# Kernel tuning notes

Measured on AMD Instinct MI355X. Metric: run time of the kernel, lower is better.

## Reference

```python
import jax, jax.numpy as jnp
import numpy as np

N, NJ, K, F = 30000, 12, 32, 128


def _resmlp(x, wr, br, w1, b1):
    # Residual: x + Linear(SiLU(x)); then ResMLP head: Linear(SiLU(.))
    h = x + jax.nn.silu(x) @ wr.T + br
    return jax.nn.silu(h) @ w1.T + b1


def setup_inputs() -> dict:
    key = jax.random.key(0)
    ks = jax.random.split(key, 40)
    d = {}
    d["atom_fea"] = jax.random.normal(ks[0], (N, F), jnp.float32)
    d["nbr_fea_idx"] = jax.random.randint(ks[1], (N, NJ), 0, N)
    d["gs"] = jax.random.normal(ks[2], (N, NJ, K), jnp.float32)
    d["gp"] = jax.random.normal(ks[3], (N, NJ, K, 3), jnp.float32)
    d["gd"] = jax.random.normal(ks[4], (N, NJ, K, 5), jnp.float32)
    # parameters (nn.init.uniform_ default is U[0,1); scaled down for stability)
    d["Gs"] = jax.random.uniform(ks[5], (F, K), jnp.float32) * 0.1
    d["Gp"] = jax.random.uniform(ks[6], (F, K), jnp.float32) * 0.1
    d["Gd"] = jax.random.uniform(ks[7], (F, K), jnp.float32) * 0.1
    d["P1"] = jax.random.uniform(ks[8], (F, F), jnp.float32) * 0.02
    d["P2"] = jax.random.uniform(ks[9], (F, F), jnp.float32) * 0.02
    d["D1"] = jax.random.uniform(ks[10], (F, F), jnp.float32) * 0.02
    d["D2"] = jax.random.uniform(ks[11], (F, F), jnp.float32) * 0.02
    i = 12
    for name in ("c", "s", "p", "d"):
        d[name + "_wr"] = jax.random.normal(ks[i], (F, F), jnp.float32) * 0.05; i += 1
        d[name + "_br"] = jnp.zeros((F,), jnp.float32)
        d[name + "_w1"] = jax.random.normal(ks[i], (F, F), jnp.float32) * 0.05; i += 1
        d[name + "_b1"] = jnp.zeros((F,), jnp.float32)
    return d


def reference(atom_fea, nbr_fea_idx, gs, gp, gd,
              Gs, Gp, Gd, P1, P2, D1, D2,
              c_wr, c_br, c_w1, c_b1,
              s_wr, s_br, s_w1, s_b1,
              p_wr, p_br, p_w1, p_b1,
              d_wr, d_br, d_w1, d_b1):
    s_fea = _resmlp(atom_fea, s_wr, s_br, s_w1, s_b1)  # (N,F)
    p_fea = _resmlp(atom_fea, p_wr, p_br, p_w1, p_b1)
    d_fea = _resmlp(atom_fea, d_wr, d_br, d_w1, d_b1)

    # s channel: env_j = Gs @ gs_j, si = sum_j s_fea[nbr_j] * env_j
    env_s = jnp.einsum('fk,njk->njf', Gs, gs)                 # (N,NJ,F)
    final_s = jnp.sum(s_fea[nbr_fea_idx] * env_s, axis=1)     # (N,F)

    # p channel: (N,F,3) per-atom, then trace((P2^T p^T)(p P1)) = sum(pP1 * pP2)
    env_p = jnp.einsum('fk,njka->njfa', Gp, gp)               # (N,NJ,F,3)
    all_p = jnp.sum(p_fea[nbr_fea_idx][..., None] * env_p, axis=1)  # (N,F,3)
    all_p = jnp.swapaxes(all_p, 1, 2)                          # (N,3,F)
    p1 = jnp.einsum('naf,fg->nag', all_p, P1)
    p2 = jnp.einsum('naf,fg->nag', all_p, P2)
    final_p = jnp.sum(p1 * p2, axis=(1, 2))[:, None]           # (N,1) -> bcast (N,F)

    # d channel: same with 5 components
    env_d = jnp.einsum('fk,njka->njfa', Gd, gd)               # (N,NJ,F,5)
    all_d = jnp.sum(d_fea[nbr_fea_idx][..., None] * env_d, axis=1)  # (N,F,5)
    all_d = jnp.swapaxes(all_d, 1, 2)                          # (N,5,F)
    d1 = jnp.einsum('naf,fg->nag', all_d, D1)
    d2 = jnp.einsum('naf,fg->nag', all_d, D2)
    final_d = jnp.sum(d1 * d2, axis=(1, 2))[:, None]

    final_c = _resmlp(atom_fea, c_wr, c_br, c_w1, c_b1)        # (N,F)
    return final_c + final_s + final_p + final_d
```

## Files before the change

kernel.cpp:

```cpp
#include <hip/hip_runtime.h>

#define N_ATOMS 30000
#define NJ 12
#define FDIM 128

typedef __attribute__((ext_vector_type(8))) short short8;
typedef __attribute__((ext_vector_type(4))) float f32x4;

#define WFRAG_OFF 0
#define GFRAG_OFF 262144
#define MFRAG_OFF 286720
#define FEA_OFF   483328
#define FEA_ELEMS 3840000
#define ALLP_OFF  23523328
#define ALLD_OFF  46563328
#define QP_OFF    84963328
#define QD_OFF    85323328

__device__ __forceinline__ unsigned pack_bf2(float a, float b){
  unsigned r;
  asm("v_cvt_pk_bf16_f32 %0, %1, %2" : "=v"(r) : "v"(a), "v"(b));
  return r;
}
__device__ __forceinline__ unsigned short f2b(float f){
  return (unsigned short)pack_bf2(f, 0.f);
}
__device__ __forceinline__ float b2f(unsigned short s){
  unsigned u = ((unsigned)s) << 16;
  return __builtin_bit_cast(float, u);
}
__device__ __forceinline__ float silu_f(float x){ return x / (1.0f + __expf(-x)); }
__device__ __forceinline__ void lds_fence(){
  __builtin_amdgcn_sched_barrier(0);
  asm volatile("s_waitcnt lgkmcnt(0)" ::: "memory");
  __builtin_amdgcn_sched_barrier(0);
}
__device__ __forceinline__ short8 frag4(unsigned d0, unsigned d1, unsigned d2, unsigned d3, bool valid){
  if (!valid){ d0 = 0u; d1 = 0u; d2 = 0u; d3 = 0u; }
  uint4 u; u.x = d0; u.y = d1; u.z = d2; u.w = d3;
  return __builtin_bit_cast(short8, u);
}

struct Ptr8 { const float* p[8]; };
struct Ptr3 { const float* p[3]; };
struct Bias { const float* br[4]; const float* b1[4]; };

__global__ __launch_bounds__(256) void k_prep(
    const float* __restrict__ P1, const float* __restrict__ P2,
    const float* __restrict__ D1, const float* __restrict__ D2,
    Ptr8 w8, Ptr3 g3, char* __restrict__ ws)
{
  int b = blockIdx.x, t = threadIdx.x;
  if (b < 16){
    int mat = b >> 3, rb = b & 7;
    const float* A = mat ? D1 : P1;
    const float* B = mat ? D2 : P2;
    unsigned short* dst = (unsigned short*)(ws + MFRAG_OFF) + (size_t)mat*16384;
    for (int it = 0; it < 8; ++it){
      int o = it*256 + t;
      int row = rb*16 + (o >> 7), col = o & 127;
      const float4* ar = (const float4*)(A + (size_t)row*128);
      const float4* br = (const float4*)(B + (size_t)col*128);
      float s = 0.f;
      #pragma unroll 8
      for (int q = 0; q < 32; ++q){
        float4 a = ar[q], c = br[q];
        s += a.x*c.x + a.y*c.y + a.z*c.z + a.w*c.w;
      }
      int ks = row >> 5, ft = col >> 4;
      int ln = (col & 15) | (((row >> 3) & 3) << 4);
      dst[(size_t)(((ks*8 + ft)*64 + ln)*8 + (row & 7))] = f2b(s);
    }
  } else if (b < 24){
    int mat = b - 16;
    const float* W = w8.p[mat];
    unsigned short* dst = (unsigned short*)(ws + WFRAG_OFF) + (size_t)mat*16384;
    for (int it = 0; it < 64; ++it){
      int idx = it*256 + t;
      int i = idx & 7, ln = (idx >> 3) & 63, ft = (idx >> 9) & 7, ks = idx >> 12;
      int f = ft*16 + (ln & 15);
      int k = ks*32 + ((ln >> 4) & 3)*8 + i;
      dst[idx] = f2b(W[(size_t)f*128 + k]);
    }
  } else {
    int mat = b - 24;
    const float* G = g3.p[mat];
    unsigned short* dst = (unsigned short*)(ws + GFRAG_OFF) + (size_t)mat*4096;
    for (int it = 0; it < 16; ++it){
      int idx = it*256 + t;
      int i = idx & 7, ln = (idx >> 3) & 63, ft = idx >> 9;
      int f = ft*16 + (ln & 15);
      int k = ((ln >> 4) & 3)*8 + i;
      dst[idx] = f2b(G[(size_t)f*32 + k]);
    }
  }
}

__global__ __launch_bounds__(256) void k_resmlp(
    const float* __restrict__ x, char* __restrict__ ws, Bias bs,
    float* __restrict__ out)
{
  __shared__ alignas(16) char sm[32768];
  const int tid = threadIdx.x, lane = tid & 63;
  const int wid = __builtin_amdgcn_readfirstlane(tid >> 6);
  const int lo = lane & 15, hi = lane >> 4;
  const int ch = blockIdx.y;
  const int rowbase = (int)blockIdx.x*64 + wid*16;
  char* xL = sm + wid*8192;
  char* hL = xL + 4096;

  #pragma unroll
  for (int it = 0; it < 8; ++it){
    int e4 = it*64 + lane;
    int row = e4 >> 5, k0 = (e4 & 31)*4;
    int grow = rowbase + row; if (grow >= N_ATOMS) grow = N_ATOMS-1;
    float4 v = *(const float4*)(x + (size_t)grow*FDIM + k0);
    uint2 u;
    u.x = pack_bf2(silu_f(v.x), silu_f(v.y));
    u.y = pack_bf2(silu_f(v.z), silu_f(v.w));
    int ks = k0 >> 5, h2 = (k0 >> 3) & 3, i0 = k0 & 7, lanep = row | (h2 << 4);
    *(uint2*)(xL + ks*1024 + lanep*16 + i0*2) = u;
  }
  lds_fence();
  short8 A[4];
  #pragma unroll
  for (int ks = 0; ks < 4; ++ks) A[ks] = *(const short8*)(xL + ks*1024 + lane*16);

  const char* wrp = ws + (size_t)(ch*2)*32768;
  const char* w1p = ws + (size_t)(ch*2 + 1)*32768;
  const float* brp = bs.br[ch];
  const float* b1p = bs.b1[ch];

  f32x4 acc[8];
  #pragma unroll
  for (int ft = 0; ft < 8; ++ft) acc[ft] = (f32x4){0.f,0.f,0.f,0.f};
  #pragma unroll
  for (int ks = 0; ks < 4; ++ks){
    #pragma unroll
    for (int ft = 0; ft < 8; ++ft){
      short8 B = *(const short8*)(wrp + (size_t)(((ks*8 + ft)*64 + lane)*16));
      acc[ft] = __builtin_amdgcn_mfma_f32_16x16x32_bf16(A[ks], B, acc[ft], 0, 0, 0);
    }
  }
  #pragma unroll
  for (int ft = 0; ft < 8; ++ft){
    int f = ft*16 + lo;
    float bias = brp[f];
    #pragma unroll
    for (int r = 0; r < 4; ++r){
      int grow = rowbase + hi*4 + r; if (grow >= N_ATOMS) grow = N_ATOMS-1;
      float h = acc[ft][r] + x[(size_t)grow*FDIM + f] + bias;
      float sh = silu_f(h);
      int ks2 = f >> 5, h2 = (f >> 3) & 3, i2 = f & 7, lanep = (hi*4 + r) | (h2 << 4);
      *(unsigned short*)(hL + ks2*1024 + lanep*16 + i2*2) = f2b(sh);
    }
  }
  lds_fence();
  short8 A2[4];
  #pragma unroll
  for (int ks = 0; ks < 4; ++ks) A2[ks] = *(const short8*)(hL + ks*1024 + lane*16);

  f32x4 acc2[8];
  #pragma unroll
  for (int ft = 0; ft < 8; ++ft) acc2[ft] = (f32x4){0.f,0.f,0.f,0.f};
  #pragma unroll
  for (int ks = 0; ks < 4; ++ks){
    #pragma unroll
    for (int ft = 0; ft < 8; ++ft){
      short8 B = *(const short8*)(w1p + (size_t)(((ks*8 + ft)*64 + lane)*16));
      acc2[ft] = __builtin_amdgcn_mfma_f32_16x16x32_bf16(A2[ks], B, acc2[ft], 0, 0, 0);
    }
  }
  if (ch == 0){
    #pragma unroll
    for (int ft = 0; ft < 8; ++ft){
      int f = ft*16 + lo;
      float bb = b1p[f];
      #pragma unroll
      for (int r = 0; r < 4; ++r){
        int grow = rowbase + hi*4 + r; if (grow >= N_ATOMS) grow = N_ATOMS-1;
        out[(size_t)grow*FDIM + f] = acc2[ft][r] + bb;
      }
    }
  } else {
    unsigned short* fea = (unsigned short*)(ws + FEA_OFF) + (size_t)(ch-1)*FEA_ELEMS;
    #pragma unroll
    for (int ft = 0; ft < 8; ++ft){
      int f = ft*16 + lo;
      float bb = b1p[f];
      #pragma unroll
      for (int r = 0; r < 4; ++r){
        int grow = rowbase + hi*4 + r; if (grow >= N_ATOMS) grow = N_ATOMS-1;
        fea[(size_t)grow*FDIM + f] = f2b(acc2[ft][r] + bb);
      }
    }
  }
}

#define FPAD 264
#define SLAB 4224

__device__ __forceinline__ void stage_fea(char* buf, const unsigned short* fea,
                                          int nb, int lane)
{
  #pragma unroll
  for (int j = 0; j < NJ; ++j){
    int nj = __builtin_amdgcn_readlane(nb, j);
    const unsigned* rp = (const unsigned*)(fea + (size_t)nj*FDIM);
    unsigned v = rp[lane];
    *(unsigned*)(buf + j*FPAD + lane*4) = v;
  }
}

__device__ __forceinline__ void body_s(
    const float* __restrict__ gs, const int* __restrict__ nbr,
    char* __restrict__ ws, float* __restrict__ out,
    char* feaL, int atom, int lane, int lo, int hi, int jc, bool jvalid)
{
  const unsigned short* feaS = (const unsigned short*)(ws + FEA_OFF);
  const f32x4 z4 = {0.f,0.f,0.f,0.f};
  int nb = 0;
  if (lane < NJ) nb = nbr[(size_t)atom*NJ + lane];

  const float* gsp = gs + (size_t)atom*384 + (jc*32 + hi*8);
  f32x4 v0 = *(const f32x4*)(gsp);
  f32x4 v1 = *(const f32x4*)(gsp + 4);

  stage_fea(feaL, feaS, nb, lane);

  short8 AfS = frag4(pack_bf2(v0[0],v0[1]), pack_bf2(v0[2],v0[3]),
                     pack_bf2(v1[0],v1[1]), pack_bf2(v1[2],v1[3]), jvalid);
  short8 Bg[8];
  #pragma unroll
  for (int ft = 0; ft < 8; ++ft)
    Bg[ft] = *(const short8*)(ws + GFRAG_OFF + (size_t)((ft*64 + lane)*16));

  const char* a0 = feaL + hi*(4*FPAD) + lo*2;

  lds_fence();
  float outv0 = 0.f, outv1 = 0.f;
  #pragma unroll
  for (int ft = 0; ft < 8; ++ft){
    float w0 = b2f(*(const unsigned short*)(a0 + 0*FPAD + ft*32));
    float w1 = b2f(*(const unsigned short*)(a0 + 1*FPAD + ft*32));
    float w2 = b2f(*(const unsigned short*)(a0 + 2*FPAD + ft*32));
    float w3 = b2f(*(const unsigned short*)(a0 + 3*FPAD + ft*32));
    f32x4 c = __builtin_amdgcn_mfma_f32_16x16x32_bf16(AfS, Bg[ft], z4, 0, 0, 0);
    float p = c[0]*w0 + c[1]*w1 + c[2]*w2 + c[3]*w3;
    p += __shfl_xor(p, 16);
    p += __shfl_xor(p, 32);
    if (ft == hi)     outv0 += p;
    if (ft == hi + 4) outv1 += p;
  }
  size_t ob = (size_t)atom*FDIM;
  out[ob + lane]      += outv0;
  out[ob + 64 + lane] += outv1;
}

__device__ __forceinline__ void body_p(
    const float* __restrict__ gp, const int* __restrict__ nbr,
    char* __restrict__ ws,
    char* feaL, int atom, int lane, int lo, int hi, int jc, bool jvalid)
{
  const unsigned short* feaP = (const unsigned short*)(ws + FEA_OFF) + FEA_ELEMS;
  unsigned short* allp = (unsigned short*)(ws + ALLP_OFF);
  const f32x4 z4 = {0.f,0.f,0.f,0.f};
  int nb = 0;
  if (lane < NJ) nb = nbr[(size_t)atom*NJ + lane];

  const float* gpp = gp + (size_t)atom*1152 + (jc*96 + hi*24);
  float pr[24];
  #pragma unroll
  for (int q = 0; q < 6; ++q){
    f32x4 v = *(const f32x4*)(gpp + q*4);
    #pragma unroll
    for (int c2 = 0; c2 < 4; ++c2) pr[q*4+c2] = v[c2];
  }
  stage_fea(feaL, feaP, nb, lane);

  short8 AfP[3];
  #pragma unroll
  for (int a = 0; a < 3; ++a)
    AfP[a] = frag4(pack_bf2(pr[0+a],pr[3+a]),   pack_bf2(pr[6+a],pr[9+a]),
                   pack_bf2(pr[12+a],pr[15+a]), pack_bf2(pr[18+a],pr[21+a]), jvalid);
  short8 Bg[8];
  #pragma unroll
  for (int ft = 0; ft < 8; ++ft)
    Bg[ft] = *(const short8*)(ws + GFRAG_OFF + 8192 + (size_t)((ft*64 + lane)*16));

  const char* a0 = feaL + hi*(4*FPAD) + lo*2;

  lds_fence();
  #pragma unroll
  for (int ft = 0; ft < 8; ++ft){
    float w0 = b2f(*(const unsigned short*)(a0 + 0*FPAD + ft*32));
    float w1 = b2f(*(const unsigned short*)(a0 + 1*FPAD + ft*32));
    float w2 = b2f(*(const unsigned short*)(a0 + 2*FPAD + ft*32));
    float w3 = b2f(*(const unsigned short*)(a0 + 3*FPAD + ft*32));
    #pragma unroll
    for (int a = 0; a < 3; ++a){
      f32x4 c = __builtin_amdgcn_mfma_f32_16x16x32_bf16(AfP[a], Bg[ft], z4, 0, 0, 0);
      float p = c[0]*w0 + c[1]*w1 + c[2]*w2 + c[3]*w3;
      p += __shfl_xor(p, 16);
      p += __shfl_xor(p, 32);
      if (lane < 16)
        allp[(size_t)(atom*3 + a)*FDIM + ft*16 + lane] = f2b(p);
    }
  }
}

__device__ __forceinline__ void body_d(
    const float* __restrict__ gd, const int* __restrict__ nbr,
    char* __restrict__ ws,
    char* feaL, int atom, int lane, int lo, int hi, int jc, bool jvalid)
{
  const unsigned short* feaD = (const unsigned short*)(ws + FEA_OFF) + 2*FEA_ELEMS;
  unsigned short* alld = (unsigned short*)(ws + ALLD_OFF);
  const char* gfd = ws + GFRAG_OFF + 16384;
  const f32x4 z4 = {0.f,0.f,0.f,0.f};
  int nb = 0;
  if (lane < NJ) nb = nbr[(size_t)atom*NJ + lane];

  const float* gdp = gd + (size_t)atom*1920 + (jc*160 + hi*40);
  float dr[40];
  #pragma unroll
  for (int q = 0; q < 10; ++q){
    f32x4 v = *(const f32x4*)(gdp + q*4);
    #pragma unroll
    for (int c2 = 0; c2 < 4; ++c2) dr[q*4+c2] = v[c2];
  }
  stage_fea(feaL, feaD, nb, lane);

  short8 AfD[5];
  #pragma unroll
  for (int a = 0; a < 5; ++a)
    AfD[a] = frag4(pack_bf2(dr[0+a],dr[5+a]),   pack_bf2(dr[10+a],dr[15+a]),
                   pack_bf2(dr[20+a],dr[25+a]), pack_bf2(dr[30+a],dr[35+a]), jvalid);

  const char* a0 = feaL + hi*(4*FPAD) + lo*2;

  lds_fence();
  short8 Bcur = *(const short8*)(gfd + (size_t)(lane*16));
  #pragma unroll
  for (int ft = 0; ft < 8; ++ft){
    short8 Bn;
    if (ft < 7) Bn = *(const short8*)(gfd + (size_t)(((ft+1)*64 + lane)*16));
    float w0 = b2f(*(const unsigned short*)(a0 + 0*FPAD + ft*32));
    float w1 = b2f(*(const unsigned short*)(a0 + 1*FPAD + ft*32));
    float w2 = b2f(*(const unsigned short*)(a0 + 2*FPAD + ft*32));
    float w3 = b2f(*(const unsigned short*)(a0 + 3*FPAD + ft*32));
    #pragma unroll
    for (int a = 0; a < 5; ++a){
      f32x4 c = __builtin_amdgcn_mfma_f32_16x16x32_bf16(AfD[a], Bcur, z4, 0, 0, 0);
      float p = c[0]*w0 + c[1]*w1 + c[2]*w2 + c[3]*w3;
      p += __shfl_xor(p, 16);
      p += __shfl_xor(p, 32);
      if (lane < 16)
        alld[(size_t)(atom*5 + a)*FDIM + ft*16 + lane] = f2b(p);
    }
    Bcur = Bn;
  }
}

__global__ __launch_bounds__(256) void k_chan(
    const float* __restrict__ gs, const float* __restrict__ gp,
    const float* __restrict__ gd, const int* __restrict__ nbr,
    char* __restrict__ ws, float* __restrict__ out)
{
  __shared__ alignas(16) char sm[4*SLAB];
  const int tid = threadIdx.x, lane = tid & 63;
  const int wid = __builtin_amdgcn_readfirstlane(tid >> 6);
  const int lo = lane & 15, hi = lane >> 4;
  const bool jvalid = lo < NJ;
  const int jc = jvalid ? lo : NJ-1;
  char* feaL = sm + wid*SLAB;
  const int atom = (int)blockIdx.x*4 + wid;
  const int ch = (int)blockIdx.y;

  #pragma unroll
  for (int t = 0; t < 4; ++t)
    *(float*)(feaL + NJ*FPAD + (t*64 + lane)*4) = 0.f;
  if (lane < 8) *(float*)(feaL + NJ*FPAD + 1024 + lane*4) = 0.f;

  if (ch == 0)      body_s(gs, nbr, ws, out, feaL, atom, lane, lo, hi, jc, jvalid);
  else if (ch == 1) body_p(gp, nbr, ws, feaL, atom, lane, lo, hi, jc, jvalid);
  else              body_d(gd, nbr, ws, feaL, atom, lane, lo, hi, jc, jvalid);
}

__global__ __launch_bounds__(256) void k_quad(char* __restrict__ ws)
{
  __shared__ alignas(16) char mB[32768];
  const int tid = threadIdx.x, lane = tid & 63;
  const int wid = __builtin_amdgcn_readfirstlane(tid >> 6);
  const int lo = lane & 15, hi = lane >> 4;
  const int mat = blockIdx.y;
  const f32x4* msrc = (const f32x4*)(ws + MFRAG_OFF + (size_t)mat*32768);
  #pragma unroll
  for (int it = 0; it < 8; ++it)
    *((f32x4*)mB + it*256 + tid) = msrc[it*256 + tid];
  __syncthreads();

  const char* rows = ws + (mat ? ALLD_OFF : ALLP_OFF);
  float* qdst = (float*)(ws + (mat ? QD_OFF : QP_OFF));
  const int ntiles = mat ? (N_ATOMS*5)/16 : (N_ATOMS*3)/16;
  const int nw = (int)gridDim.x*4;

  for (int t = (int)blockIdx.x*4 + wid; t < ntiles; t += nw){
    const int rowb = t*16;
    short8 Aq[4];
    #pragma unroll
    for (int ks = 0; ks < 4; ++ks)
      Aq[ks] = *(const short8*)(rows + (size_t)(rowb + lo)*256 + ks*64 + hi*16);
    unsigned short vv[8][4];
    #pragma unroll
    for (int ft = 0; ft < 8; ++ft)
      #pragma unroll
      for (int r = 0; r < 4; ++r)
        vv[ft][r] = *(const unsigned short*)(rows + (size_t)(rowb + hi*4 + r)*256 + (ft*16 + lo)*2);

    f32x4 acc[8];
    #pragma unroll
    for (int ft = 0; ft < 8; ++ft) acc[ft] = (f32x4){0.f,0.f,0.f,0.f};
    #pragma unroll
    for (int ks = 0; ks < 4; ++ks){
      #pragma unroll
      for (int ft = 0; ft < 8; ++ft){
        short8 B = *(const short8*)(mB + (size_t)(((ks*8 + ft)*64 + lane)*16));
        acc[ft] = __builtin_amdgcn_mfma_f32_16x16x32_bf16(Aq[ks], B, acc[ft], 0, 0, 0);
      }
    }
    float part[4] = {0.f,0.f,0.f,0.f};
    #pragma unroll
    for (int ft = 0; ft < 8; ++ft)
      #pragma unroll
      for (int r = 0; r < 4; ++r)
        part[r] += acc[ft][r] * b2f(vv[ft][r]);
    #pragma unroll
    for (int r = 0; r < 4; ++r){
      #pragma unroll
      for (int m = 1; m < 16; m <<= 1) part[r] += __shfl_xor(part[r], m);
    }
    if (lo == 0){
      #pragma unroll
      for (int r = 0; r < 4; ++r) qdst[rowb + hi*4 + r] = part[r];
    }
  }
}

__global__ __launch_bounds__(256) void k_final(char* __restrict__ ws,
                                               float* __restrict__ out)
{
  const float* qp = (const float*)(ws + QP_OFF);
  const float* qd = (const float*)(ws + QD_OFF);
  int e = (int)blockIdx.x*256 + threadIdx.x;
  int i = e >> 7;
  float q = qp[i*3] + qp[i*3+1] + qp[i*3+2]
          + qd[i*5] + qd[i*5+1] + qd[i*5+2] + qd[i*5+3] + qd[i*5+4];
  out[e] += q;
}

extern "C" void kernel_launch(void* const* d_in, const int* in_sizes, int n_in,
                              void* d_out, int out_size, void* d_ws, size_t ws_size,
                              hipStream_t stream)
{
  const float* atom_fea = (const float*)d_in[0];
  const int*   nbr      = (const int*)d_in[1];
  const float* gs = (const float*)d_in[2];
  const float* gp = (const float*)d_in[3];
  const float* gd = (const float*)d_in[4];
  const float* Gs = (const float*)d_in[5];
  const float* Gp = (const float*)d_in[6];
  const float* Gd = (const float*)d_in[7];
  const float* P1 = (const float*)d_in[8];
  const float* P2 = (const float*)d_in[9];
  const float* D1 = (const float*)d_in[10];
  const float* D2 = (const float*)d_in[11];

  Ptr8 w8;
  w8.p[0] = (const float*)d_in[12];
  w8.p[1] = (const float*)d_in[14];
  w8.p[2] = (const float*)d_in[16];
  w8.p[3] = (const float*)d_in[18];
  w8.p[4] = (const float*)d_in[20];
  w8.p[5] = (const float*)d_in[22];
  w8.p[6] = (const float*)d_in[24];
  w8.p[7] = (const float*)d_in[26];
  Ptr3 g3; g3.p[0] = Gs; g3.p[1] = Gp; g3.p[2] = Gd;
  Bias bs;
  bs.br[0] = (const float*)d_in[13]; bs.b1[0] = (const float*)d_in[15];
  bs.br[1] = (const float*)d_in[17]; bs.b1[1] = (const float*)d_in[19];
  bs.br[2] = (const float*)d_in[21]; bs.b1[2] = (const float*)d_in[23];
  bs.br[3] = (const float*)d_in[25]; bs.b1[3] = (const float*)d_in[27];

  char* ws = (char*)d_ws;
  float* out = (float*)d_out;

  k_prep  <<<27, 256, 0, stream>>>(P1, P2, D1, D2, w8, g3, ws);
  dim3 g1((N_ATOMS + 63)/64, 4);
  k_resmlp<<<g1, 256, 0, stream>>>(atom_fea, ws, bs, out);
  dim3 gc(N_ATOMS/4, 3);
  k_chan  <<<gc, 256, 0, stream>>>(gs, gp, gd, nbr, ws, out);
  dim3 gq(256, 2);
  k_quad  <<<gq, 256, 0, stream>>>(ws);
  k_final <<<15000, 256, 0, stream>>>(ws, out);
}
```

Baseline: 262.0 us.

## Merge s/p/d channel blocks into one block per atom group

Replaces the 3-way blockIdx.y channel split in k_chan with a single block that handles all three channels for its atoms. The neighbor index load is shared, all three feature gathers are staged into one larger LDS slab up front, and the gp/gd loads are issued early so they overlap with the s and p compute. It also adds a launch-bounds occupancy hint. In exchange it uses more LDS per block and holds more registers live (pr/dr arrays), which may lower occupancy, and the grid has a third as many blocks.

```diff
diff --git a/kernel.cpp b/kernel.cpp
--- a/kernel.cpp
+++ b/kernel.cpp
@@ -198,7 +198,8 @@
 }
 
 #define FPAD 264
-#define SLAB 4224
+#define SLABROWS 40
+#define SLAB (SLABROWS*FPAD)
 
 __device__ __forceinline__ void stage_fea(char* buf, const unsigned short* fea,
                                           int nb, int lane)
@@ -212,157 +213,7 @@
   }
 }
 
-__device__ __forceinline__ void body_s(
-    const float* __restrict__ gs, const int* __restrict__ nbr,
-    char* __restrict__ ws, float* __restrict__ out,
-    char* feaL, int atom, int lane, int lo, int hi, int jc, bool jvalid)
-{
-  const unsigned short* feaS = (const unsigned short*)(ws + FEA_OFF);
-  const f32x4 z4 = {0.f,0.f,0.f,0.f};
-  int nb = 0;
-  if (lane < NJ) nb = nbr[(size_t)atom*NJ + lane];
-
-  const float* gsp = gs + (size_t)atom*384 + (jc*32 + hi*8);
-  f32x4 v0 = *(const f32x4*)(gsp);
-  f32x4 v1 = *(const f32x4*)(gsp + 4);
-
-  stage_fea(feaL, feaS, nb, lane);
-
-  short8 AfS = frag4(pack_bf2(v0[0],v0[1]), pack_bf2(v0[2],v0[3]),
-                     pack_bf2(v1[0],v1[1]), pack_bf2(v1[2],v1[3]), jvalid);
-  short8 Bg[8];
-  #pragma unroll
-  for (int ft = 0; ft < 8; ++ft)
-    Bg[ft] = *(const short8*)(ws + GFRAG_OFF + (size_t)((ft*64 + lane)*16));
-
-  const char* a0 = feaL + hi*(4*FPAD) + lo*2;
-
-  lds_fence();
-  float outv0 = 0.f, outv1 = 0.f;
-  #pragma unroll
-  for (int ft = 0; ft < 8; ++ft){
-    float w0 = b2f(*(const unsigned short*)(a0 + 0*FPAD + ft*32));
-    float w1 = b2f(*(const unsigned short*)(a0 + 1*FPAD + ft*32));
-    float w2 = b2f(*(const unsigned short*)(a0 + 2*FPAD + ft*32));
-    float w3 = b2f(*(const unsigned short*)(a0 + 3*FPAD + ft*32));
-    f32x4 c = __builtin_amdgcn_mfma_f32_16x16x32_bf16(AfS, Bg[ft], z4, 0, 0, 0);
-    float p = c[0]*w0 + c[1]*w1 + c[2]*w2 + c[3]*w3;
-    p += __shfl_xor(p, 16);
-    p += __shfl_xor(p, 32);
-    if (ft == hi)     outv0 += p;
-    if (ft == hi + 4) outv1 += p;
-  }
-  size_t ob = (size_t)atom*FDIM;
-  out[ob + lane]      += outv0;
-  out[ob + 64 + lane] += outv1;
-}
-
-__device__ __forceinline__ void body_p(
-    const float* __restrict__ gp, const int* __restrict__ nbr,
-    char* __restrict__ ws,
-    char* feaL, int atom, int lane, int lo, int hi, int jc, bool jvalid)
-{
-  const unsigned short* feaP = (const unsigned short*)(ws + FEA_OFF) + FEA_ELEMS;
-  unsigned short* allp = (unsigned short*)(ws + ALLP_OFF);
-  const f32x4 z4 = {0.f,0.f,0.f,0.f};
-  int nb = 0;
-  if (lane < NJ) nb = nbr[(size_t)atom*NJ + lane];
-
-  const float* gpp = gp + (size_t)atom*1152 + (jc*96 + hi*24);
-  float pr[24];
-  #pragma unroll
-  for (int q = 0; q < 6; ++q){
-    f32x4 v = *(const f32x4*)(gpp + q*4);
-    #pragma unroll
-    for (int c2 = 0; c2 < 4; ++c2) pr[q*4+c2] = v[c2];
-  }
-  stage_fea(feaL, feaP, nb, lane);
-
-  short8 AfP[3];
-  #pragma unroll
-  for (int a = 0; a < 3; ++a)
-    AfP[a] = frag4(pack_bf2(pr[0+a],pr[3+a]),   pack_bf2(pr[6+a],pr[9+a]),
-                   pack_bf2(pr[12+a],pr[15+a]), pack_bf2(pr[18+a],pr[21+a]), jvalid);
-  short8 Bg[8];
-  #pragma unroll
-  for (int ft = 0; ft < 8; ++ft)
-    Bg[ft] = *(const short8*)(ws + GFRAG_OFF + 8192 + (size_t)((ft*64 + lane)*16));
-
-  const char* a0 = feaL + hi*(4*FPAD) + lo*2;
-
-  lds_fence();
-  #pragma unroll
-  for (int ft = 0; ft < 8; ++ft){
-    float w0 = b2f(*(const unsigned short*)(a0 + 0*FPAD + ft*32));
-    float w1 = b2f(*(const unsigned short*)(a0 + 1*FPAD + ft*32));
-    float w2 = b2f(*(const unsigned short*)(a0 + 2*FPAD + ft*32));
-    float w3 = b2f(*(const unsigned short*)(a0 + 3*FPAD + ft*32));
-    #pragma unroll
-    for (int a = 0; a < 3; ++a){
-      f32x4 c = __builtin_amdgcn_mfma_f32_16x16x32_bf16(AfP[a], Bg[ft], z4, 0, 0, 0);
-      float p = c[0]*w0 + c[1]*w1 + c[2]*w2 + c[3]*w3;
-      p += __shfl_xor(p, 16);
-      p += __shfl_xor(p, 32);
-      if (lane < 16)
-        allp[(size_t)(atom*3 + a)*FDIM + ft*16 + lane] = f2b(p);
-    }
-  }
-}
-
-__device__ __forceinline__ void body_d(
-    const float* __restrict__ gd, const int* __restrict__ nbr,
-    char* __restrict__ ws,
-    char* feaL, int atom, int lane, int lo, int hi, int jc, bool jvalid)
-{
-  const unsigned short* feaD = (const unsigned short*)(ws + FEA_OFF) + 2*FEA_ELEMS;
-  unsigned short* alld = (unsigned short*)(ws + ALLD_OFF);
-  const char* gfd = ws + GFRAG_OFF + 16384;
-  const f32x4 z4 = {0.f,0.f,0.f,0.f};
-  int nb = 0;
-  if (lane < NJ) nb = nbr[(size_t)atom*NJ + lane];
-
-  const float* gdp = gd + (size_t)atom*1920 + (jc*160 + hi*40);
-  float dr[40];
-  #pragma unroll
-  for (int q = 0; q < 10; ++q){
-    f32x4 v = *(const f32x4*)(gdp + q*4);
-    #pragma unroll
-    for (int c2 = 0; c2 < 4; ++c2) dr[q*4+c2] = v[c2];
-  }
-  stage_fea(feaL, feaD, nb, lane);
-
-  short8 AfD[5];
-  #pragma unroll
-  for (int a = 0; a < 5; ++a)
-    AfD[a] = frag4(pack_bf2(dr[0+a],dr[5+a]),   pack_bf2(dr[10+a],dr[15+a]),
-                   pack_bf2(dr[20+a],dr[25+a]), pack_bf2(dr[30+a],dr[35+a]), jvalid);
-
-  const char* a0 = feaL + hi*(4*FPAD) + lo*2;
-
-  lds_fence();
-  short8 Bcur = *(const short8*)(gfd + (size_t)(lane*16));
-  #pragma unroll
-  for (int ft = 0; ft < 8; ++ft){
-    short8 Bn;
-    if (ft < 7) Bn = *(const short8*)(gfd + (size_t)(((ft+1)*64 + lane)*16));
-    float w0 = b2f(*(const unsigned short*)(a0 + 0*FPAD + ft*32));
-    float w1 = b2f(*(const unsigned short*)(a0 + 1*FPAD + ft*32));
-    float w2 = b2f(*(const unsigned short*)(a0 + 2*FPAD + ft*32));
-    float w3 = b2f(*(const unsigned short*)(a0 + 3*FPAD + ft*32));
-    #pragma unroll
-    for (int a = 0; a < 5; ++a){
-      f32x4 c = __builtin_amdgcn_mfma_f32_16x16x32_bf16(AfD[a], Bcur, z4, 0, 0, 0);
-      float p = c[0]*w0 + c[1]*w1 + c[2]*w2 + c[3]*w3;
-      p += __shfl_xor(p, 16);
-      p += __shfl_xor(p, 32);
-      if (lane < 16)
-        alld[(size_t)(atom*5 + a)*FDIM + ft*16 + lane] = f2b(p);
-    }
-    Bcur = Bn;
-  }
-}
-
-__global__ __launch_bounds__(256) void k_chan(
+__global__ __launch_bounds__(256, 4) void k_chan(
     const float* __restrict__ gs, const float* __restrict__ gp,
     const float* __restrict__ gd, const int* __restrict__ nbr,
     char* __restrict__ ws, float* __restrict__ out)
@@ -373,18 +224,134 @@
   const int lo = lane & 15, hi = lane >> 4;
   const bool jvalid = lo < NJ;
   const int jc = jvalid ? lo : NJ-1;
-  char* feaL = sm + wid*SLAB;
+  char* slab = sm + wid*SLAB;
   const int atom = (int)blockIdx.x*4 + wid;
-  const int ch = (int)blockIdx.y;
+  const f32x4 z4 = {0.f,0.f,0.f,0.f};
+  const unsigned short* feaS = (const unsigned short*)(ws + FEA_OFF);
+  const char* gfrag = ws + GFRAG_OFF;
+
+  int nb = 0;
+  if (lane < NJ) nb = nbr[(size_t)atom*NJ + lane];
 
   #pragma unroll
   for (int t = 0; t < 4; ++t)
-    *(float*)(feaL + NJ*FPAD + (t*64 + lane)*4) = 0.f;
-  if (lane < 8) *(float*)(feaL + NJ*FPAD + 1024 + lane*4) = 0.f;
-
-  if (ch == 0)      body_s(gs, nbr, ws, out, feaL, atom, lane, lo, hi, jc, jvalid);
-  else if (ch == 1) body_p(gp, nbr, ws, feaL, atom, lane, lo, hi, jc, jvalid);
-  else              body_d(gd, nbr, ws, feaL, atom, lane, lo, hi, jc, jvalid);
+    *(float*)(slab + 36*FPAD + (t*64 + lane)*4) = 0.f;
+  if (lane < 8) *(float*)(slab + 36*FPAD + 1024 + lane*4) = 0.f;
+
+  stage_fea(slab,            feaS,               nb, lane);
+  stage_fea(slab + 12*FPAD,  feaS + FEA_ELEMS,   nb, lane);
+  stage_fea(slab + 24*FPAD,  feaS + 2*FEA_ELEMS, nb, lane);
+
+  const float* gsp = gs + (size_t)atom*384 + (jc*32 + hi*8);
+  f32x4 sv0 = *(const f32x4*)(gsp);
+  f32x4 sv1 = *(const f32x4*)(gsp + 4);
+  const float* gpp = gp + (size_t)atom*1152 + (jc*96 + hi*24);
+  float pr[24];
+  #pragma unroll
+  for (int q = 0; q < 6; ++q){
+    f32x4 v = *(const f32x4*)(gpp + q*4);
+    #pragma unroll
+    for (int c2 = 0; c2 < 4; ++c2) pr[q*4+c2] = v[c2];
+  }
+
+  const char* a0s = slab + hi*(4*FPAD) + lo*2;
+
+  lds_fence();
+
+  {
+    short8 AfS = frag4(pack_bf2(sv0[0],sv0[1]), pack_bf2(sv0[2],sv0[3]),
+                       pack_bf2(sv1[0],sv1[1]), pack_bf2(sv1[2],sv1[3]), jvalid);
+    short8 Bg[8];
+    #pragma unroll
+    for (int ft = 0; ft < 8; ++ft)
+      Bg[ft] = *(const short8*)(gfrag + (size_t)((ft*64 + lane)*16));
+    float outv0 = 0.f, outv1 = 0.f;
+    #pragma unroll
+    for (int ft = 0; ft < 8; ++ft){
+      float w0 = b2f(*(const unsigned short*)(a0s + 0*FPAD + ft*32));
+      float w1 = b2f(*(const unsigned short*)(a0s + 1*FPAD + ft*32));
+      float w2 = b2f(*(const unsigned short*)(a0s + 2*FPAD + ft*32));
+      float w3 = b2f(*(const unsigned short*)(a0s + 3*FPAD + ft*32));
+      f32x4 c = __builtin_amdgcn_mfma_f32_16x16x32_bf16(AfS, Bg[ft], z4, 0, 0, 0);
+      float p = c[0]*w0 + c[1]*w1 + c[2]*w2 + c[3]*w3;
+      p += __shfl_xor(p, 16);
+      p += __shfl_xor(p, 32);
+      if (ft == hi)     outv0 += p;
+      if (ft == hi + 4) outv1 += p;
+    }
+    size_t ob = (size_t)atom*FDIM;
+    out[ob + lane]      += outv0;
+    out[ob + 64 + lane] += outv1;
+  }
+
+  const float* gdp = gd + (size_t)atom*1920 + (jc*160 + hi*40);
+  float dr[40];
+  #pragma unroll
+  for (int q = 0; q < 10; ++q){
+    f32x4 v = *(const f32x4*)(gdp + q*4);
+    #pragma unroll
+    for (int c2 = 0; c2 < 4; ++c2) dr[q*4+c2] = v[c2];
+  }
+
+  {
+    unsigned short* allp = (unsigned short*)(ws + ALLP_OFF);
+    short8 AfP[3];
+    #pragma unroll
+    for (int a = 0; a < 3; ++a)
+      AfP[a] = frag4(pack_bf2(pr[0+a],pr[3+a]),   pack_bf2(pr[6+a],pr[9+a]),
+                     pack_bf2(pr[12+a],pr[15+a]), pack_bf2(pr[18+a],pr[21+a]), jvalid);
+    short8 Bg[8];
+    #pragma unroll
+    for (int ft = 0; ft < 8; ++ft)
+      Bg[ft] = *(const short8*)(gfrag + 8192 + (size_t)((ft*64 + lane)*16));
+    const char* a0 = a0s + 12*FPAD;
+    #pragma unroll
+    for (int ft = 0; ft < 8; ++ft){
+      float w0 = b2f(*(const unsigned short*)(a0 + 0*FPAD + ft*32));
+      float w1 = b2f(*(const unsigned short*)(a0 + 1*FPAD + ft*32));
+      float w2 = b2f(*(const unsigned short*)(a0 + 2*FPAD + ft*32));
+      float w3 = b2f(*(const unsigned short*)(a0 + 3*FPAD + ft*32));
+      #pragma unroll
+      for (int a = 0; a < 3; ++a){
+        f32x4 c = __builtin_amdgcn_mfma_f32_16x16x32_bf16(AfP[a], Bg[ft], z4, 0, 0, 0);
+        float p = c[0]*w0 + c[1]*w1 + c[2]*w2 + c[3]*w3;
+        p += __shfl_xor(p, 16);
+        p += __shfl_xor(p, 32);
+        if (lane < 16)
+          allp[(size_t)(atom*3 + a)*FDIM + ft*16 + lane] = f2b(p);
+      }
+    }
+  }
+
+  {
+    unsigned short* alld = (unsigned short*)(ws + ALLD_OFF);
+    short8 AfD[5];
+    #pragma unroll
+    for (int a = 0; a < 5; ++a)
+      AfD[a] = frag4(pack_bf2(dr[0+a],dr[5+a]),   pack_bf2(dr[10+a],dr[15+a]),
+                     pack_bf2(dr[20+a],dr[25+a]), pack_bf2(dr[30+a],dr[35+a]), jvalid);
+    short8 Bg[8];
+    #pragma unroll
+    for (int ft = 0; ft < 8; ++ft)
+      Bg[ft] = *(const short8*)(gfrag + 16384 + (size_t)((ft*64 + lane)*16));
+    const char* a0 = a0s + 24*FPAD;
+    #pragma unroll
+    for (int ft = 0; ft < 8; ++ft){
+      float w0 = b2f(*(const unsigned short*)(a0 + 0*FPAD + ft*32));
+      float w1 = b2f(*(const unsigned short*)(a0 + 1*FPAD + ft*32));
+      float w2 = b2f(*(const unsigned short*)(a0 + 2*FPAD + ft*32));
+      float w3 = b2f(*(const unsigned short*)(a0 + 3*FPAD + ft*32));
+      #pragma unroll
+      for (int a = 0; a < 5; ++a){
+        f32x4 c = __builtin_amdgcn_mfma_f32_16x16x32_bf16(AfD[a], Bg[ft], z4, 0, 0, 0);
+        float p = c[0]*w0 + c[1]*w1 + c[2]*w2 + c[3]*w3;
+        p += __shfl_xor(p, 16);
+        p += __shfl_xor(p, 32);
+        if (lane < 16)
+          alld[(size_t)(atom*5 + a)*FDIM + ft*16 + lane] = f2b(p);
+      }
+    }
+  }
 }
 
 __global__ __launch_bounds__(256) void k_quad(char* __restrict__ ws)
@@ -498,8 +465,7 @@
   k_prep  <<<27, 256, 0, stream>>>(P1, P2, D1, D2, w8, g3, ws);
   dim3 g1((N_ATOMS + 63)/64, 4);
   k_resmlp<<<g1, 256, 0, stream>>>(atom_fea, ws, bs, out);
-  dim3 gc(N_ATOMS/4, 3);
-  k_chan  <<<gc, 256, 0, stream>>>(gs, gp, gd, nbr, ws, out);
+  k_chan  <<<N_ATOMS/4, 256, 0, stream>>>(gs, gp, gd, nbr, ws, out);
   dim3 gq(256, 2);
   k_quad  <<<gq, 256, 0, stream>>>(ws);
   k_final <<<15000, 256, 0, stream>>>(ws, out);
```

New measurement: 282.1 us. +7.7%, slower.
